# Optimization experiments

Hardware: AMD Instinct MI355X
Metric: run time of the kernel (lower is better)

## Reference

```python
import jax, jax.numpy as jnp
import numpy as np

N_NODES = 50000
N_EDGES = 800000
D = 128  # hidden_channels == num_filters
SHIFT = float(np.log(2.0))


def shifted_softplus(x):
    return jax.nn.softplus(x) - SHIFT


def setup_inputs() -> dict:
    key = jax.random.key(0)
    k1, k2, k3, k4, k5 = jax.random.split(key, 5)
    v = jax.random.normal(k1, (N_NODES, D), dtype=jnp.float32)
    e = jax.random.normal(k2, (N_EDGES, D), dtype=jnp.float32)
    edge_index = jax.random.randint(k3, (2, N_EDGES), 0, N_NODES, dtype=jnp.int64)
    # Xavier-uniform weights, zero biases (as in reset_parameters)
    limit = float(np.sqrt(6.0 / (D + D)))
    W1 = jax.random.uniform(k4, (D, D), minval=-limit, maxval=limit, dtype=jnp.float32)
    b1 = jnp.zeros((D,), dtype=jnp.float32)
    W2 = jax.random.uniform(k5, (D, D), minval=-limit, maxval=limit, dtype=jnp.float32)
    b2 = jnp.zeros((D,), dtype=jnp.float32)
    return {"v": v, "e": e, "edge_index": edge_index,
            "W1": W1, "b1": b1, "W2": W2, "b2": b2}


def reference(v, e, edge_index, W1, b1, W2, b2):
    i = edge_index[1]  # destination node per edge, [E]
    # scatter-sum edge messages into nodes: [N, D]
    agg = jax.ops.segment_sum(e, i, num_segments=v.shape[0])
    h = shifted_softplus(agg @ W1.T + b1)  # lin1 + act (dropout = identity)
    out = h @ W2.T + b2                    # lin2
    return v + out
```

## Files before the change

kernel.cpp:

```cpp
#include <hip/hip_runtime.h>
#include <cstdint>
#include <cstddef>

#define D 128
#define CAP 64

static __device__ __forceinline__ float ssp(float x) {
    float ax = fabsf(x);
    return fmaxf(x, 0.0f) + log1pf(__expf(-ax)) - 0.6931471805599453f;
}

__global__ void build_lists(const int* __restrict__ ei, int E,
                            int* __restrict__ cnt, int* __restrict__ slots) {
    int t = blockIdx.x * blockDim.x + threadIdx.x;
    if (t < E) {
        int dst = ei[E + t];
        int slot = atomicAdd(&cnt[dst], 1);
        if (slot < CAP) slots[(size_t)dst * CAP + slot] = t;
    }
}

__global__ void transpose_w(const float* __restrict__ W1, const float* __restrict__ W2,
                            float* __restrict__ WT1, float* __restrict__ WT2) {
    const float* W  = blockIdx.y ? W2 : W1;
    float*       WT = blockIdx.y ? WT2 : WT1;
    int j = blockIdx.x;
    int k = threadIdx.x;
    WT[k * D + j] = W[j * D + k];
}

static __device__ __forceinline__ void fma4x4(const float4 a, const float4 w0,
                                              const float4 w1, const float4 w2,
                                              const float4 w3, float4& c) {
    c.x = fmaf(a.x, w0.x, fmaf(a.y, w1.x, fmaf(a.z, w2.x, fmaf(a.w, w3.x, c.x))));
    c.y = fmaf(a.x, w0.y, fmaf(a.y, w1.y, fmaf(a.z, w2.y, fmaf(a.w, w3.y, c.y))));
    c.z = fmaf(a.x, w0.z, fmaf(a.y, w1.z, fmaf(a.z, w2.z, fmaf(a.w, w3.z, c.z))));
    c.w = fmaf(a.x, w0.w, fmaf(a.y, w1.w, fmaf(a.z, w2.w, fmaf(a.w, w3.w, c.w))));
}

__global__ __launch_bounds__(256) void fused_gather_mlp(
    const float* __restrict__ e, const int* __restrict__ cnt,
    const int* __restrict__ slots, const float* __restrict__ vin,
    const float* __restrict__ WT1, const float* __restrict__ b1,
    const float* __restrict__ WT2, const float* __restrict__ b2,
    float* __restrict__ out, int N) {
    __shared__ float As[32][D];
    __shared__ float Hs[32][D];
    const int tid  = threadIdx.x;
    const int row0 = blockIdx.x * 32;
    const int wave = tid >> 6;
    const int lane = tid & 63;
    const int half = lane >> 5;
    const int l32  = lane & 31;

    for (int r = wave; r < 32; r += 4) {
        int n = row0 + r;
        float4 s0 = make_float4(0.f, 0.f, 0.f, 0.f);
        float4 s1 = make_float4(0.f, 0.f, 0.f, 0.f);
        float4 s2 = make_float4(0.f, 0.f, 0.f, 0.f);
        float4 s3 = make_float4(0.f, 0.f, 0.f, 0.f);
        if (n < N) {
            int c = cnt[n];
            if (c > CAP) c = CAP;
            const int* sl = slots + (size_t)n * CAP;
            int myEid = sl[lane < c ? lane : 0];
            int j = 0;
            for (; j + 8 <= c; j += 8) {
                int e0 = __shfl(myEid, j + 0 + half);
                int e1 = __shfl(myEid, j + 2 + half);
                int e2 = __shfl(myEid, j + 4 + half);
                int e3 = __shfl(myEid, j + 6 + half);
                float4 x0 = ((const float4*)(e + (size_t)e0 * D))[l32];
                float4 x1 = ((const float4*)(e + (size_t)e1 * D))[l32];
                float4 x2 = ((const float4*)(e + (size_t)e2 * D))[l32];
                float4 x3 = ((const float4*)(e + (size_t)e3 * D))[l32];
                s0.x += x0.x; s0.y += x0.y; s0.z += x0.z; s0.w += x0.w;
                s1.x += x1.x; s1.y += x1.y; s1.z += x1.z; s1.w += x1.w;
                s2.x += x2.x; s2.y += x2.y; s2.z += x2.z; s2.w += x2.w;
                s3.x += x3.x; s3.y += x3.y; s3.z += x3.z; s3.w += x3.w;
            }
            for (; j < c; j += 2) {
                int i0 = j + half;
                int e0 = __shfl(myEid, i0 < c ? i0 : 0);
                float w = (i0 < c) ? 1.f : 0.f;
                float4 x0 = ((const float4*)(e + (size_t)e0 * D))[l32];
                s0.x = fmaf(w, x0.x, s0.x);
                s0.y = fmaf(w, x0.y, s0.y);
                s0.z = fmaf(w, x0.z, s0.z);
                s0.w = fmaf(w, x0.w, s0.w);
            }
        }
        float4 t4;
        t4.x = (s0.x + s1.x) + (s2.x + s3.x);
        t4.y = (s0.y + s1.y) + (s2.y + s3.y);
        t4.z = (s0.z + s1.z) + (s2.z + s3.z);
        t4.w = (s0.w + s1.w) + (s2.w + s3.w);
        t4.x += __shfl(t4.x, l32 + 32);
        t4.y += __shfl(t4.y, l32 + 32);
        t4.z += __shfl(t4.z, l32 + 32);
        t4.w += __shfl(t4.w, l32 + 32);
        if (half == 0) ((float4*)(&As[r][0]))[l32] = t4;
    }
    __syncthreads();

    const int jg = (tid & 31) << 2;
    const int rg = (tid >> 5) << 2;

    float4 acc[4];
    #pragma unroll
    for (int r = 0; r < 4; ++r) acc[r] = make_float4(0.f, 0.f, 0.f, 0.f);

    for (int k = 0; k < D; k += 4) {
        float4 w0 = *(const float4*)(WT1 + (k + 0) * D + jg);
        float4 w1 = *(const float4*)(WT1 + (k + 1) * D + jg);
        float4 w2 = *(const float4*)(WT1 + (k + 2) * D + jg);
        float4 w3 = *(const float4*)(WT1 + (k + 3) * D + jg);
        #pragma unroll
        for (int r = 0; r < 4; ++r) {
            float4 a = *(const float4*)(&As[rg + r][k]);
            fma4x4(a, w0, w1, w2, w3, acc[r]);
        }
    }
    {
        float4 bb = *(const float4*)(b1 + jg);
        #pragma unroll
        for (int r = 0; r < 4; ++r) {
            float4 h;
            h.x = ssp(acc[r].x + bb.x);
            h.y = ssp(acc[r].y + bb.y);
            h.z = ssp(acc[r].z + bb.z);
            h.w = ssp(acc[r].w + bb.w);
            *(float4*)(&Hs[rg + r][jg]) = h;
        }
    }
    __syncthreads();

    #pragma unroll
    for (int r = 0; r < 4; ++r) acc[r] = make_float4(0.f, 0.f, 0.f, 0.f);

    for (int k = 0; k < D; k += 4) {
        float4 w0 = *(const float4*)(WT2 + (k + 0) * D + jg);
        float4 w1 = *(const float4*)(WT2 + (k + 1) * D + jg);
        float4 w2 = *(const float4*)(WT2 + (k + 2) * D + jg);
        float4 w3 = *(const float4*)(WT2 + (k + 3) * D + jg);
        #pragma unroll
        for (int r = 0; r < 4; ++r) {
            float4 a = *(const float4*)(&Hs[rg + r][k]);
            fma4x4(a, w0, w1, w2, w3, acc[r]);
        }
    }
    {
        float4 bb = *(const float4*)(b2 + jg);
        #pragma unroll
        for (int r = 0; r < 4; ++r) {
            int row = row0 + rg + r;
            if (row < N) {
                float4 vv = *(const float4*)(vin + (size_t)row * D + jg);
                float4 o;
                o.x = vv.x + acc[r].x + bb.x;
                o.y = vv.y + acc[r].y + bb.y;
                o.z = vv.z + acc[r].z + bb.z;
                o.w = vv.w + acc[r].w + bb.w;
                *(float4*)(out + (size_t)row * D + jg) = o;
            }
        }
    }
}

extern "C" void kernel_launch(void* const* d_in, const int* in_sizes, int n_in,
                              void* d_out, int out_size, void* d_ws, size_t ws_size,
                              hipStream_t stream) {
    const float* v  = (const float*)d_in[0];
    const float* e  = (const float*)d_in[1];
    const int*   ei = (const int*)d_in[2];
    const float* W1 = (const float*)d_in[3];
    const float* b1 = (const float*)d_in[4];
    const float* W2 = (const float*)d_in[5];
    const float* b2 = (const float*)d_in[6];

    const int N = in_sizes[0] / D;
    const int E = in_sizes[1] / D;

    char*  ws  = (char*)d_ws;
    size_t off = 0;
    auto alloc = [&](size_t bytes) {
        void* p = ws + off;
        off += (bytes + 255) & ~(size_t)255;
        return p;
    };
    int*   cnt   = (int*)alloc((size_t)N * 4);
    int*   slots = (int*)alloc((size_t)N * CAP * 4);
    float* WT1   = (float*)alloc((size_t)D * D * 4);
    float* WT2   = (float*)alloc((size_t)D * D * 4);
    (void)ws_size; (void)n_in; (void)out_size;

    hipMemsetAsync(cnt, 0, (size_t)N * sizeof(int), stream);
    build_lists<<<(E + 255) / 256, 256, 0, stream>>>(ei, E, cnt, slots);
    transpose_w<<<dim3(D, 2), D, 0, stream>>>(W1, W2, WT1, WT2);
    fused_gather_mlp<<<(N + 31) / 32, 256, 0, stream>>>(
        e, cnt, slots, v, WT1, b1, WT2, b2, (float*)d_out, N);
}
```

Measured before the change: 687.8 us.

## Gather each node with half-wave, nontemporal edge loads, wider unroll

The gather phase now assigns one 32-lane half-wave per destination node instead of a full wave, so two nodes are processed per wave and the final cross-half shuffle reduction is removed. Edge ids are loaded as int2 per lane and fetched with width-32 shuffles. Edge rows are read with nontemporal loads to avoid polluting cache, the main loop unrolls 8 edges per iteration, and the tail handles 4 edges per step. This aims for more memory-level parallelism per wave in the bandwidth-bound gather, at the cost of more registers and masked tail loads.

```diff
diff --git a/kernel.cpp b/kernel.cpp
--- a/kernel.cpp
+++ b/kernel.cpp
@@ -4,6 +4,8 @@
 
 #define D 128
 #define CAP 64
+
+typedef float f4v __attribute__((ext_vector_type(4)));
 
 static __device__ __forceinline__ float ssp(float x) {
     float ax = fabsf(x);
@@ -36,6 +38,15 @@
     c.y = fmaf(a.x, w0.y, fmaf(a.y, w1.y, fmaf(a.z, w2.y, fmaf(a.w, w3.y, c.y))));
     c.z = fmaf(a.x, w0.z, fmaf(a.y, w1.z, fmaf(a.z, w2.z, fmaf(a.w, w3.z, c.z))));
     c.w = fmaf(a.x, w0.w, fmaf(a.y, w1.w, fmaf(a.z, w2.w, fmaf(a.w, w3.w, c.w))));
+}
+
+static __device__ __forceinline__ int pickEid(const int2 eid2, int idx) {
+    int v = (idx & 1) ? eid2.y : eid2.x;
+    return __shfl(v, idx >> 1, 32);
+}
+
+static __device__ __forceinline__ f4v ldnt(const float* p) {
+    return __builtin_nontemporal_load((const f4v*)p);
 }
 
 __global__ __launch_bounds__(256) void fused_gather_mlp(
@@ -48,58 +59,60 @@
     __shared__ float Hs[32][D];
     const int tid  = threadIdx.x;
     const int row0 = blockIdx.x * 32;
-    const int wave = tid >> 6;
-    const int lane = tid & 63;
-    const int half = lane >> 5;
-    const int l32  = lane & 31;
-
-    for (int r = wave; r < 32; r += 4) {
-        int n = row0 + r;
-        float4 s0 = make_float4(0.f, 0.f, 0.f, 0.f);
-        float4 s1 = make_float4(0.f, 0.f, 0.f, 0.f);
-        float4 s2 = make_float4(0.f, 0.f, 0.f, 0.f);
-        float4 s3 = make_float4(0.f, 0.f, 0.f, 0.f);
+    const int half = tid >> 5;
+    const int l32  = tid & 31;
+
+    for (int r = half; r < 32; r += 8) {
+        const int n = row0 + r;
+        f4v s0 = 0.f, s1 = 0.f, s2 = 0.f, s3 = 0.f;
         if (n < N) {
             int c = cnt[n];
             if (c > CAP) c = CAP;
-            const int* sl = slots + (size_t)n * CAP;
-            int myEid = sl[lane < c ? lane : 0];
+            const int2 eid2 = ((const int2*)(slots + (size_t)n * CAP))[l32];
             int j = 0;
             for (; j + 8 <= c; j += 8) {
-                int e0 = __shfl(myEid, j + 0 + half);
-                int e1 = __shfl(myEid, j + 2 + half);
-                int e2 = __shfl(myEid, j + 4 + half);
-                int e3 = __shfl(myEid, j + 6 + half);
-                float4 x0 = ((const float4*)(e + (size_t)e0 * D))[l32];
-                float4 x1 = ((const float4*)(e + (size_t)e1 * D))[l32];
-                float4 x2 = ((const float4*)(e + (size_t)e2 * D))[l32];
-                float4 x3 = ((const float4*)(e + (size_t)e3 * D))[l32];
-                s0.x += x0.x; s0.y += x0.y; s0.z += x0.z; s0.w += x0.w;
-                s1.x += x1.x; s1.y += x1.y; s1.z += x1.z; s1.w += x1.w;
-                s2.x += x2.x; s2.y += x2.y; s2.z += x2.z; s2.w += x2.w;
-                s3.x += x3.x; s3.y += x3.y; s3.z += x3.z; s3.w += x3.w;
+                int e0 = pickEid(eid2, j + 0);
+                int e1 = pickEid(eid2, j + 1);
+                int e2 = pickEid(eid2, j + 2);
+                int e3 = pickEid(eid2, j + 3);
+                int e4 = pickEid(eid2, j + 4);
+                int e5 = pickEid(eid2, j + 5);
+                int e6 = pickEid(eid2, j + 6);
+                int e7 = pickEid(eid2, j + 7);
+                f4v x0 = ldnt(e + (size_t)e0 * D + l32 * 4);
+                f4v x1 = ldnt(e + (size_t)e1 * D + l32 * 4);
+                f4v x2 = ldnt(e + (size_t)e2 * D + l32 * 4);
+                f4v x3 = ldnt(e + (size_t)e3 * D + l32 * 4);
+                f4v x4 = ldnt(e + (size_t)e4 * D + l32 * 4);
+                f4v x5 = ldnt(e + (size_t)e5 * D + l32 * 4);
+                f4v x6 = ldnt(e + (size_t)e6 * D + l32 * 4);
+                f4v x7 = ldnt(e + (size_t)e7 * D + l32 * 4);
+                s0 += x0; s1 += x1; s2 += x2; s3 += x3;
+                s0 += x4; s1 += x5; s2 += x6; s3 += x7;
             }
-            for (; j < c; j += 2) {
-                int i0 = j + half;
-                int e0 = __shfl(myEid, i0 < c ? i0 : 0);
-                float w = (i0 < c) ? 1.f : 0.f;
-                float4 x0 = ((const float4*)(e + (size_t)e0 * D))[l32];
-                s0.x = fmaf(w, x0.x, s0.x);
-                s0.y = fmaf(w, x0.y, s0.y);
-                s0.z = fmaf(w, x0.z, s0.z);
-                s0.w = fmaf(w, x0.w, s0.w);
+            for (; j < c; j += 4) {
+                const int  i1 = (j + 1 < c) ? j + 1 : j;
+                const int  i2 = (j + 2 < c) ? j + 2 : j;
+                const int  i3 = (j + 3 < c) ? j + 3 : j;
+                const float w1 = (j + 1 < c) ? 1.f : 0.f;
+                const float w2 = (j + 2 < c) ? 1.f : 0.f;
+                const float w3 = (j + 3 < c) ? 1.f : 0.f;
+                int e0 = pickEid(eid2, j);
+                int e1 = pickEid(eid2, i1);
+                int e2 = pickEid(eid2, i2);
+                int e3 = pickEid(eid2, i3);
+                f4v x0 = ldnt(e + (size_t)e0 * D + l32 * 4);
+                f4v x1 = ldnt(e + (size_t)e1 * D + l32 * 4);
+                f4v x2 = ldnt(e + (size_t)e2 * D + l32 * 4);
+                f4v x3 = ldnt(e + (size_t)e3 * D + l32 * 4);
+                s0 += x0;
+                s1 += x1 * w1;
+                s2 += x2 * w2;
+                s3 += x3 * w3;
             }
         }
-        float4 t4;
-        t4.x = (s0.x + s1.x) + (s2.x + s3.x);
-        t4.y = (s0.y + s1.y) + (s2.y + s3.y);
-        t4.z = (s0.z + s1.z) + (s2.z + s3.z);
-        t4.w = (s0.w + s1.w) + (s2.w + s3.w);
-        t4.x += __shfl(t4.x, l32 + 32);
-        t4.y += __shfl(t4.y, l32 + 32);
-        t4.z += __shfl(t4.z, l32 + 32);
-        t4.w += __shfl(t4.w, l32 + 32);
-        if (half == 0) ((float4*)(&As[r][0]))[l32] = t4;
+        f4v t4 = (s0 + s1) + (s2 + s3);
+        *((f4v*)(&As[r][0]) + l32) = t4;
     }
     __syncthreads();
 
```

New measurement: 662.8 us. -3.6%, faster.
